# Kernel tuning notes

Measured on AMD Instinct MI355X. Metric: run time of the kernel, lower is better.

Reference implementation:

```python
import jax, jax.numpy as jnp
import numpy as np

HDIM = 1024
CDIM = 256
TEMPER = 10.0
IGNORE_OUT = 0.0
EPS = 1e-6


def setup_inputs() -> dict:
    key = jax.random.key(0)
    ks = jax.random.split(key, 6)
    B, T, D = 2, 128, 384
    x = jax.random.normal(ks[0], (B, T, D), jnp.float32)
    y = jax.random.normal(ks[1], (B, T, D), jnp.float32)
    # xavier-normal style init for the two linear layers
    W_enc = jax.random.normal(ks[2], (D, HDIM), jnp.float32) * np.sqrt(2.0 / (D + HDIM))
    b_enc = jnp.zeros((HDIM,), jnp.float32)
    W_dec = jax.random.normal(ks[3], (HDIM, D), jnp.float32) * np.sqrt(2.0 / (D + HDIM))
    b_dec = jnp.zeros((D,), jnp.float32)
    return {"x": x, "y": y, "W_enc": W_enc, "b_enc": b_enc, "W_dec": W_dec, "b_dec": b_dec}


def reference(x, y, W_enc, b_enc, W_dec, b_dec):
    B, T, D = x.shape
    n_iter = HDIM // CDIM
    pad = D - 1
    # shift_idx[s, j] = s + j : window of width D at offset s, s in [0, 2D-2]
    shift_idx = jnp.arange(2 * D - 1)[:, None] + jnp.arange(D)[None, :]

    seq_mask = (y == IGNORE_OUT)                       # (B,T,D) bool
    denom_seq = jnp.sum(~seq_mask).astype(x.dtype)
    qn = jnp.linalg.norm(y, axis=-1)                   # (B,T)

    mask_prev = None
    x_dis, losses = [], []
    for _ in range(n_iter):
        # --- _pad_for_shift: (B,T,2D-1,D) shifted windows of x ---
        kp = jnp.pad(x, ((0, 0), (0, 0), (pad, pad)))  # (B,T,3D-2)
        kpt = kp[..., shift_idx]                       # (B,T,2D-1,D)
        # --- _score (cos) + argmax over shifts ---
        kn = jnp.linalg.norm(kpt, axis=-1)             # (B,T,2D-1)
        sim = jnp.einsum('btsd,btd->bts', kpt, y) / (qn[..., None] * kn + EPS)
        sim = jnp.where(jnp.isnan(sim), 0.0, sim)
        theta = jnp.argmax(sim, axis=-1)               # (B,T) int
        x_opt = jnp.take_along_axis(kpt, theta[..., None, None], axis=-2)[..., 0, :]  # (B,T,D)
        # --- attention: elementwise cos-scaled score, temp softmax, detached ---
        dn = (jnp.linalg.norm(x_opt, axis=-1, keepdims=True)
              * jnp.linalg.norm(y, axis=-1, keepdims=True) + EPS)
        attn = jax.nn.softmax((x_opt * y / dn) / TEMPER, axis=-1)
        attn = jnp.where(jnp.isnan(attn), 0.0, attn)
        attn = jax.lax.stop_gradient(attn)
        x_attn = x_opt * attn
        # --- _reverse_pad_for_shift: window at offset 2D-2-theta ---
        kp2 = jnp.pad(x_attn, ((0, 0), (0, 0), (pad, pad)))
        rev_idx = (2 * D - 2 - theta)[..., None] + jnp.arange(D)  # (B,T,D)
        x_ele = jnp.take_along_axis(kp2, rev_idx, axis=-1)         # (B,T,D)
        # --- self_net: encoder -> top-k sparsify -> decoder_self ---
        h = x_ele @ W_enc + b_enc                      # (B,T,HDIM)
        if mask_prev is not None:
            h = jnp.where(mask_prev > 0, 1e-10, h)
        _, idx_top = jax.lax.top_k(h, CDIM)            # (B,T,CDIM)
        flat = idx_top.reshape(B * T, CDIM)
        mask_cur = jnp.zeros((B * T, HDIM), x.dtype).at[
            jnp.arange(B * T)[:, None], flat].set(1.0).reshape(B, T, HDIM)
        if mask_prev is None:
            mask_prev = mask_cur
        else:
            mask_prev = mask_prev + mask_cur - mask_prev * mask_cur
        h = h * mask_cur
        out = h @ W_dec + b_dec                        # (B,T,D)
        x_dis.append(out)
        # --- SeqLoss (masked MSE, mean-reduced by count of valid elems) ---
        err = jnp.where(seq_mask, 0.0, (out - x) ** 2) / denom_seq
        losses.append(jnp.sum(err))
    return jnp.stack(x_dis), jnp.stack(losses)
```

## Files before the change

### kernel.cpp

```cpp
#include <hip/hip_runtime.h>
#include <math.h>

#define DD 384
#define HD 1024
#define CD 256
#define NS 765
#define NITER 4
#define NROWS 256
#define TEMPER_F 10.0f
#define EPSF 1e-6f
#define CUTF 1e-10f

typedef unsigned long long u64;
typedef unsigned int u32;

__device__ __forceinline__ u32 flipf(float f) {
    u32 u = __float_as_uint(f);
    return u ^ ((u32)((int)u >> 31) | 0x80000000u);
}
__device__ __forceinline__ float unflipf(u32 s) {
    u32 fl = ~s;
    u32 u = (fl & 0x80000000u) ? (fl ^ 0x80000000u) : ~fl;
    return __uint_as_float(u);
}
__device__ __forceinline__ u64 shflx64(u64 v, int m) {
    int lo = __shfl_xor((int)(u32)v, m, 64);
    int hi = __shfl_xor((int)(u32)(v >> 32), m, 64);
    return ((u64)(u32)hi << 32) | (u32)lo;
}
__device__ __forceinline__ u32 bf16r(float f) {
    u32 u = __float_as_uint(f);
    return (u + 0x7FFFu + ((u >> 16) & 1u)) >> 16;
}
__device__ __forceinline__ u32 pack2(float a, float b) {
    return bf16r(a) | (bf16r(b) << 16);
}
__device__ __forceinline__ float blo(u32 p) { return __uint_as_float(p << 16); }
__device__ __forceinline__ float bhi(u32 p) { return __uint_as_float(p & 0xFFFF0000u); }

__global__ __launch_bounds__(256) void convert_kernel(
    const float* __restrict__ We, const float* __restrict__ Wd,
    uint2* __restrict__ we16, uint2* __restrict__ wd16)
{
    const int t = blockIdx.x * 256 + threadIdx.x;
    for (int i = t; i < (DD * HD) / 4; i += 65536) {
        float4 v = ((const float4*)We)[i];
        we16[i] = make_uint2(pack2(v.x, v.y), pack2(v.z, v.w));
    }
    for (int i = t; i < (HD * DD) / 4; i += 65536) {
        float4 v = ((const float4*)Wd)[i];
        wd16[i] = make_uint2(pack2(v.x, v.y), pack2(v.z, v.w));
    }
}

__global__ __launch_bounds__(512) void fused_kernel(
    const float* __restrict__ x, const float* __restrict__ y,
    const u32* __restrict__ wenc16, const float* __restrict__ benc,
    const u32* __restrict__ wdec16, const float* __restrict__ bdec,
    float* __restrict__ out_xdis, float* __restrict__ lossp,
    int* __restrict__ ycnt)
{
    const int row  = blockIdx.x;
    const int tid  = threadIdx.x;
    const int lane = tid & 63;
    const int wid  = tid >> 6;

    __shared__ __align__(16) float xpad[1152];
    __shared__ __align__(16) float yr[DD];
    __shared__ float xa[DD];
    __shared__ __align__(16) float xe_s[DD];
    __shared__ __align__(16) float hpart[HD];
    __shared__ __align__(16) u64   skey[HD];
    __shared__ __align__(16) uint2 dec2[HD];
    __shared__ float wred[8];
    __shared__ int   wredi[8];
    __shared__ float wredn[8];
    __shared__ float s_sc[4];
    __shared__ int   s_theta, s_fb;
    __shared__ float loss4[NITER];

    const float* xrow = x + row * DD;
    const float* yrow = y + row * DD;

    for (int i = tid; i < 1152; i += 512)
        xpad[i] = (i >= DD - 1 && i < 2 * DD - 1) ? xrow[i - (DD - 1)] : 0.f;
    if (tid < DD) yr[tid] = yrow[tid];
    __syncthreads();

    if (tid < DD) {
        float p = yr[tid] * yr[tid];
        int   c = (yr[tid] != 0.f) ? 1 : 0;
        for (int o = 32; o; o >>= 1) {
            p += __shfl_xor(p, o, 64);
            c += __shfl_xor(c, o, 64);
        }
        if (lane == 0) { wred[wid] = p; wredi[wid] = c; }
    }
    __syncthreads();
    if (tid == 0) {
        float s = 0.f; int c = 0;
        for (int w = 0; w < 6; ++w) { s += wred[w]; c += wredi[w]; }
        s_sc[0] = sqrtf(s);
        ycnt[row] = c;
    }
    __syncthreads();
    const float qn = s_sc[0];

    float bv = -INFINITY; int bs = 0x7fffffff; float bn = 0.f;
    if (tid < 192) {
        const float4* xp4 = (const float4*)xpad;
        const float4* yp4 = (const float4*)yr;
        float4 A = xp4[tid];
        const float f0 = A.x * A.x, f1 = A.y * A.y, f2 = A.z * A.z;
        float d0 = 0.f, d1 = 0.f, d2 = 0.f, d3 = 0.f, n0 = 0.f;
#pragma unroll 4
        for (int jc = 0; jc < 96; ++jc) {
            float4 B = xp4[tid + jc + 1];
            float4 Y = yp4[jc];
            d0 += A.x * Y.x; d0 += A.y * Y.y; d0 += A.z * Y.z; d0 += A.w * Y.w;
            d1 += A.y * Y.x; d1 += A.z * Y.y; d1 += A.w * Y.z; d1 += B.x * Y.w;
            d2 += A.z * Y.x; d2 += A.w * Y.y; d2 += B.x * Y.z; d2 += B.y * Y.w;
            d3 += A.w * Y.x; d3 += B.x * Y.y; d3 += B.y * Y.z; d3 += B.z * Y.w;
            n0 += A.x * A.x; n0 += A.y * A.y; n0 += A.z * A.z; n0 += A.w * A.w;
            A = B;
        }
        const float n1 = n0 - f0 + A.x * A.x;
        const float n2 = n1 - f1 + A.y * A.y;
        const float n3 = n2 - f2 + A.z * A.z;
        const int s0 = 4 * tid;
        float sim0 = d0 / (qn * sqrtf(n0) + EPSF);
        float sim1 = d1 / (qn * sqrtf(n1) + EPSF);
        float sim2 = d2 / (qn * sqrtf(n2) + EPSF);
        float sim3 = d3 / (qn * sqrtf(n3) + EPSF);
        bv = sim0; bs = s0; bn = n0;
        if (s0 + 1 < NS && sim1 > bv) { bv = sim1; bs = s0 + 1; bn = n1; }
        if (s0 + 2 < NS && sim2 > bv) { bv = sim2; bs = s0 + 2; bn = n2; }
        if (s0 + 3 < NS && sim3 > bv) { bv = sim3; bs = s0 + 3; bn = n3; }
    }
    for (int o = 32; o; o >>= 1) {
        float v2 = __shfl_xor(bv, o, 64);
        int   i2 = __shfl_xor(bs, o, 64);
        float n2 = __shfl_xor(bn, o, 64);
        if (v2 > bv || (v2 == bv && i2 < bs)) { bv = v2; bs = i2; bn = n2; }
    }
    if (lane == 0) { wred[wid] = bv; wredi[wid] = bs; wredn[wid] = bn; }
    __syncthreads();
    if (tid == 0) {
        float v = wred[0]; int b = wredi[0]; float nn = wredn[0];
        for (int w = 1; w < 8; ++w)
            if (wred[w] > v || (wred[w] == v && wredi[w] < b)) {
                v = wred[w]; b = wredi[w]; nn = wredn[w];
            }
        s_theta = b;
        s_sc[1] = sqrtf(nn) * qn + EPSF;
    }
    __syncthreads();
    const int theta = s_theta;
    const float dn = s_sc[1];

    float xo = 0.f, z = 0.f;
    if (tid < DD) {
        xo = xpad[theta + tid];
        z = (xo * yr[tid] / dn) / TEMPER_F;
        float m = z;
        for (int o = 32; o; o >>= 1) { float w2 = __shfl_xor(m, o, 64); if (w2 > m) m = w2; }
        if (lane == 0) wred[wid] = m;
    }
    __syncthreads();
    if (tid == 0) {
        float m = wred[0];
        for (int w = 1; w < 6; ++w) if (wred[w] > m) m = wred[w];
        s_sc[2] = m;
    }
    __syncthreads();
    float ez = 0.f;
    if (tid < DD) {
        ez = expf(z - s_sc[2]);
        float p = ez;
        for (int o = 32; o; o >>= 1) p += __shfl_xor(p, o, 64);
        if (lane == 0) wred[wid] = p;
    }
    __syncthreads();
    if (tid == 0) {
        float s = 0.f;
        for (int w = 0; w < 6; ++w) s += wred[w];
        s_sc[3] = s;
    }
    __syncthreads();
    if (tid < DD) xa[tid] = xo * (ez / s_sc[3]);
    __syncthreads();
    if (tid < DD) {
        int sj = tid - (theta - (DD - 1));
        xe_s[tid] = (sj >= 0 && sj < DD) ? xa[sj] : 0.f;
    }
    __syncthreads();

    const int c4 = tid & 255;
    const int jh = tid >> 8;
    float4 acc = make_float4(0.f, 0.f, 0.f, 0.f);
    {
        const u32* wbase = wenc16 + (size_t)(jh * 192) * 512 + 2 * c4;
        const float* xb = xe_s + jh * 192;
#pragma unroll 8
        for (int j = 0; j < 192; ++j) {
            float xv = xb[j];
            uint2 wv = *(const uint2*)(wbase + (size_t)j * 512);
            acc.x += xv * blo(wv.x); acc.y += xv * bhi(wv.x);
            acc.z += xv * blo(wv.y); acc.w += xv * bhi(wv.y);
        }
    }
    if (jh == 1) *(float4*)&hpart[4 * c4] = acc;
    if (tid == 0) s_fb = HD;
    if (tid < NITER) loss4[tid] = 0.f;
    __syncthreads();
    if (jh == 0) {
        float4 hp = *(const float4*)&hpart[4 * c4];
        float4 bb = *(const float4*)&benc[4 * c4];
        hp.x += acc.x + bb.x;
        hp.y += acc.y + bb.y;
        hp.z += acc.z + bb.z;
        hp.w += acc.w + bb.w;
        *(float4*)&hpart[4 * c4] = hp;
    }
    __syncthreads();

    float2 hh = *(const float2*)&hpart[2 * tid];
    u64 e0 = ((u64)(~flipf(hh.x)) << 32) | (u32)(2 * tid);
    u64 e1 = ((u64)(~flipf(hh.y)) << 32) | (u32)(2 * tid + 1);

    for (int k = 2; k <= HD; k <<= 1) {
        const bool up = ((2 * tid) & k) == 0;
        for (int j = k >> 1; j > 0; j >>= 1) {
            if (j == 1) {
                bool sw = up ? (e0 > e1) : (e0 < e1);
                if (sw) { u64 t2 = e0; e0 = e1; e1 = t2; }
            } else if (j <= 64) {
                const int m = j >> 1;
                u64 p0 = shflx64(e0, m);
                u64 p1 = shflx64(e1, m);
                const bool takeMin = (((tid & m) == 0) == up);
                e0 = takeMin ? (e0 < p0 ? e0 : p0) : (e0 > p0 ? e0 : p0);
                e1 = takeMin ? (e1 < p1 ? e1 : p1) : (e1 > p1 ? e1 : p1);
            } else {
                __syncthreads();
                skey[2 * tid]     = e0;
                skey[2 * tid + 1] = e1;
                __syncthreads();
                const int tp = tid ^ (j >> 1);
                u64 p0 = skey[2 * tp];
                u64 p1 = skey[2 * tp + 1];
                const bool takeMin = (((tid & (j >> 1)) == 0) == up);
                e0 = takeMin ? (e0 < p0 ? e0 : p0) : (e0 > p0 ? e0 : p0);
                e1 = takeMin ? (e1 < p1 ? e1 : p1) : (e1 > p1 ? e1 : p1);
            }
        }
    }

    {
        float v0 = unflipf((u32)(e0 >> 32));
        float v1 = unflipf((u32)(e1 >> 32));
        dec2[2 * tid]     = make_uint2(__float_as_uint(v0), ((u32)e0) * 192);
        dec2[2 * tid + 1] = make_uint2(__float_as_uint(v1), ((u32)e1) * 192);
        int fbloc = HD;
        if (!(v1 > CUTF)) fbloc = 2 * tid + 1;
        if (!(v0 > CUTF)) fbloc = 2 * tid;
        for (int o = 32; o; o >>= 1) { int t2 = __shfl_xor(fbloc, o, 64); if (t2 < fbloc) fbloc = t2; }
        if (lane == 0) atomicMin(&s_fb, fbloc);
    }
    __syncthreads();
    const int fb = s_fb;

    {
        const int k = tid >> 7;
        const int g = tid & 127;
        const bool active = (g < 96);
        int n = 0;
        if (active) {
            n = (k == 0) ? CD : fb - k * CD;
            if (n < 0) n = 0; if (n > CD) n = CD;
        }
        float4 oacc = make_float4(0.f, 0.f, 0.f, 0.f);
        if (active) oacc = *(const float4*)&bdec[4 * g];
        const u32* wd = wdec16 + 2 * g;
        const int base = k * CD;
        int r = 0;
        for (; r + 8 <= n; r += 8) {
#pragma unroll
            for (int q = 0; q < 8; q += 2) {
                uint4 dv = *(const uint4*)&dec2[base + r + q];
                float v0 = __uint_as_float(dv.x);
                uint2 w0 = *(const uint2*)(wd + dv.y);
                float v1 = __uint_as_float(dv.z);
                uint2 w1 = *(const uint2*)(wd + dv.w);
                oacc.x += v0 * blo(w0.x); oacc.y += v0 * bhi(w0.x);
                oacc.z += v0 * blo(w0.y); oacc.w += v0 * bhi(w0.y);
                oacc.x += v1 * blo(w1.x); oacc.y += v1 * bhi(w1.x);
                oacc.z += v1 * blo(w1.y); oacc.w += v1 * bhi(w1.y);
            }
        }
        for (; r < n; ++r) {
            uint2 dv = dec2[base + r];
            float v0 = __uint_as_float(dv.x);
            uint2 w0 = *(const uint2*)(wd + dv.y);
            oacc.x += v0 * blo(w0.x); oacc.y += v0 * bhi(w0.x);
            oacc.z += v0 * blo(w0.y); oacc.w += v0 * bhi(w0.y);
        }
        float l = 0.f;
        if (active) {
            *(float4*)&out_xdis[((size_t)k * NROWS + row) * DD + 4 * g] = oacc;
            float4 xv = *(const float4*)&xrow[4 * g];
            float4 yv = *(const float4*)&yr[4 * g];
            float e;
            e = oacc.x - xv.x; if (yv.x != 0.f) l += e * e;
            e = oacc.y - xv.y; if (yv.y != 0.f) l += e * e;
            e = oacc.z - xv.z; if (yv.z != 0.f) l += e * e;
            e = oacc.w - xv.w; if (yv.w != 0.f) l += e * e;
        }
        for (int o = 32; o; o >>= 1) l += __shfl_xor(l, o, 64);
        if (lane == 0) atomicAdd(&loss4[k], l);
    }
    __syncthreads();
    if (tid < NITER) lossp[row * NITER + tid] = loss4[tid];
}

__global__ __launch_bounds__(256) void finalize2(
    const float* __restrict__ lossp, const int* __restrict__ ycnt,
    float* __restrict__ losses)
{
    const int tid = threadIdx.x, lane = tid & 63, w = tid >> 6;
    __shared__ int ctot[4];
    int c = ycnt[tid];
    for (int o = 32; o; o >>= 1) c += __shfl_xor(c, o, 64);
    if (lane == 0) ctot[w] = c;
    __syncthreads();
    const int total = ctot[0] + ctot[1] + ctot[2] + ctot[3];
    float s = lossp[lane * NITER + w] + lossp[(lane + 64) * NITER + w]
            + lossp[(lane + 128) * NITER + w] + lossp[(lane + 192) * NITER + w];
    for (int o = 32; o; o >>= 1) s += __shfl_xor(s, o, 64);
    if (lane == 0) losses[w] = s / (float)total;
}

extern "C" void kernel_launch(void* const* d_in, const int* in_sizes, int n_in,
                              void* d_out, int out_size, void* d_ws, size_t ws_size,
                              hipStream_t stream) {
    const float* x    = (const float*)d_in[0];
    const float* y    = (const float*)d_in[1];
    const float* Wenc = (const float*)d_in[2];
    const float* benc = (const float*)d_in[3];
    const float* Wdec = (const float*)d_in[4];
    const float* bdec = (const float*)d_in[5];

    float* out  = (float*)d_out;
    float* loss = out + (out_size - NITER);

    float* lossp  = (float*)d_ws;
    int*   ycnt   = (int*)(lossp + NROWS * NITER);
    u32*   wenc16 = (u32*)(ycnt + NROWS);
    u32*   wdec16 = wenc16 + (DD * HD) / 2;

    convert_kernel<<<256, 256, 0, stream>>>(Wenc, Wdec, (uint2*)wenc16, (uint2*)wdec16);
    fused_kernel<<<NROWS, 512, 0, stream>>>(x, y, wenc16, benc, wdec16, bdec,
                                            out, lossp, ycnt);
    finalize2<<<1, 256, 0, stream>>>(lossp, ycnt, loss);
}
```

Before: 111.3 us.

## Double block size to 1024 threads, splitting encoder K and sort per element

Launches the fused per-row kernel with 1024 threads instead of 512. The encoder matvec splits K into four 96-long slices reduced through shared memory, the bitonic top-k sort holds one key per thread instead of two, and the decoder gives each thread two output columns instead of four. The aim is more parallelism per row, since only 256 blocks run on a large GPU and per-thread serial work dominates. In exchange there are more barriers, more shared-memory reduction traffic and higher register pressure under the 1024-thread launch bound. Parts of the sort-stage code and the argmax reduction setup are not visible, so whether every phase was adjusted for 16 wavefronts cannot be confirmed.

```diff
diff --git a/kernel.cpp b/kernel.cpp
--- a/kernel.cpp
+++ b/kernel.cpp
@@ -53,7 +53,7 @@
     }
 }
 
-__global__ __launch_bounds__(512) void fused_kernel(
+__global__ __launch_bounds__(1024) void fused_kernel(
     const float* __restrict__ x, const float* __restrict__ y,
     const u32* __restrict__ wenc16, const float* __restrict__ benc,
     const u32* __restrict__ wdec16, const float* __restrict__ bdec,
@@ -69,12 +69,12 @@
     __shared__ __align__(16) float yr[DD];
     __shared__ float xa[DD];
     __shared__ __align__(16) float xe_s[DD];
-    __shared__ __align__(16) float hpart[HD];
+    __shared__ __align__(16) float part[4][HD];
     __shared__ __align__(16) u64   skey[HD];
     __shared__ __align__(16) uint2 dec2[HD];
-    __shared__ float wred[8];
-    __shared__ int   wredi[8];
-    __shared__ float wredn[8];
+    __shared__ float wred[16];
+    __shared__ int   wredi[16];
+    __shared__ float wredn[16];
     __shared__ float s_sc[4];
     __shared__ int   s_theta, s_fb;
     __shared__ float loss4[NITER];
@@ -82,7 +82,7 @@
     const float* xrow = x + row * DD;
     const float* yrow = y + row * DD;
 
-    for (int i = tid; i < 1152; i += 512)
+    for (int i = tid; i < 1152; i += 1024)
         xpad[i] = (i >= DD - 1 && i < 2 * DD - 1) ? xrow[i - (DD - 1)] : 0.f;
     if (tid < DD) yr[tid] = yrow[tid];
     __syncthreads();
@@ -147,7 +147,7 @@
     __syncthreads();
     if (tid == 0) {
         float v = wred[0]; int b = wredi[0]; float nn = wredn[0];
-        for (int w = 1; w < 8; ++w)
+        for (int w = 1; w < 16; ++w)
             if (wred[w] > v || (wred[w] == v && wredi[w] < b)) {
                 v = wred[w]; b = wredi[w]; nn = wredn[w];
             }
@@ -195,75 +195,54 @@
     }
     __syncthreads();
 
-    const int c4 = tid & 255;
-    const int jh = tid >> 8;
-    float4 acc = make_float4(0.f, 0.f, 0.f, 0.f);
     {
-        const u32* wbase = wenc16 + (size_t)(jh * 192) * 512 + 2 * c4;
-        const float* xb = xe_s + jh * 192;
+        const int ks = tid >> 8;
+        const int c4 = tid & 255;
+        const u32* wbase = wenc16 + (size_t)(ks * 96) * 512 + 2 * c4;
+        const float* xb = xe_s + ks * 96;
+        float4 acc = make_float4(0.f, 0.f, 0.f, 0.f);
 #pragma unroll 8
-        for (int j = 0; j < 192; ++j) {
+        for (int j = 0; j < 96; ++j) {
             float xv = xb[j];
             uint2 wv = *(const uint2*)(wbase + (size_t)j * 512);
             acc.x += xv * blo(wv.x); acc.y += xv * bhi(wv.x);
             acc.z += xv * blo(wv.y); acc.w += xv * bhi(wv.y);
         }
-    }
-    if (jh == 1) *(float4*)&hpart[4 * c4] = acc;
+        *(float4*)&part[ks][4 * c4] = acc;
+    }
     if (tid == 0) s_fb = HD;
     if (tid < NITER) loss4[tid] = 0.f;
     __syncthreads();
-    if (jh == 0) {
-        float4 hp = *(const float4*)&hpart[4 * c4];
-        float4 bb = *(const float4*)&benc[4 * c4];
-        hp.x += acc.x + bb.x;
-        hp.y += acc.y + bb.y;
-        hp.z += acc.z + bb.z;
-        hp.w += acc.w + bb.w;
-        *(float4*)&hpart[4 * c4] = hp;
-    }
-    __syncthreads();
-
-    float2 hh = *(const float2*)&hpart[2 * tid];
-    u64 e0 = ((u64)(~flipf(hh.x)) << 32) | (u32)(2 * tid);
-    u64 e1 = ((u64)(~flipf(hh.y)) << 32) | (u32)(2 * tid + 1);
+
+    u64 e;
+    {
+        float hv = part[0][tid] + part[1][tid] + part[2][tid] + part[3][tid]
+                 + benc[tid];
+        e = ((u64)(~flipf(hv)) << 32) | (u32)tid;
+    }
 
     for (int k = 2; k <= HD; k <<= 1) {
-        const bool up = ((2 * tid) & k) == 0;
+        const bool up = (tid & k) == 0;
         for (int j = k >> 1; j > 0; j >>= 1) {
-            if (j == 1) {
-                bool sw = up ? (e0 > e1) : (e0 < e1);
-                if (sw) { u64 t2 = e0; e0 = e1; e1 = t2; }
-            } else if (j <= 64) {
-                const int m = j >> 1;
-                u64 p0 = shflx64(e0, m);
-                u64 p1 = shflx64(e1, m);
-                const bool takeMin = (((tid & m) == 0) == up);
-                e0 = takeMin ? (e0 < p0 ? e0 : p0) : (e0 > p0 ? e0 : p0);
-                e1 = takeMin ? (e1 < p1 ? e1 : p1) : (e1 > p1 ? e1 : p1);
+            if (j <= 32) {
+                u64 p = shflx64(e, j);
+                const bool takeMin = ((tid & j) == 0) == up;
+                e = takeMin ? (e < p ? e : p) : (e > p ? e : p);
             } else {
                 __syncthreads();
-                skey[2 * tid]     = e0;
-                skey[2 * tid + 1] = e1;
+                skey[tid] = e;
                 __syncthreads();
-                const int tp = tid ^ (j >> 1);
-                u64 p0 = skey[2 * tp];
-                u64 p1 = skey[2 * tp + 1];
-                const bool takeMin = (((tid & (j >> 1)) == 0) == up);
-                e0 = takeMin ? (e0 < p0 ? e0 : p0) : (e0 > p0 ? e0 : p0);
-                e1 = takeMin ? (e1 < p1 ? e1 : p1) : (e1 > p1 ? e1 : p1);
+                u64 p = skey[tid ^ j];
+                const bool takeMin = ((tid & j) == 0) == up;
+                e = takeMin ? (e < p ? e : p) : (e > p ? e : p);
             }
         }
     }
 
     {
-        float v0 = unflipf((u32)(e0 >> 32));
-        float v1 = unflipf((u32)(e1 >> 32));
-        dec2[2 * tid]     = make_uint2(__float_as_uint(v0), ((u32)e0) * 192);
-        dec2[2 * tid + 1] = make_uint2(__float_as_uint(v1), ((u32)e1) * 192);
-        int fbloc = HD;
-        if (!(v1 > CUTF)) fbloc = 2 * tid + 1;
-        if (!(v0 > CUTF)) fbloc = 2 * tid;
+        float v = unflipf((u32)(e >> 32));
+        dec2[tid] = make_uint2(__float_as_uint(v), ((u32)e) * 192);
+        int fbloc = (v > CUTF) ? HD : tid;
         for (int o = 32; o; o >>= 1) { int t2 = __shfl_xor(fbloc, o, 64); if (t2 < fbloc) fbloc = t2; }
         if (lane == 0) atomicMin(&s_fb, fbloc);
     }
@@ -271,17 +250,17 @@
     const int fb = s_fb;
 
     {
-        const int k = tid >> 7;
-        const int g = tid & 127;
-        const bool active = (g < 96);
+        const int k = tid >> 8;
+        const int g = tid & 255;
+        const bool active = (g < 192);
         int n = 0;
         if (active) {
             n = (k == 0) ? CD : fb - k * CD;
             if (n < 0) n = 0; if (n > CD) n = CD;
         }
-        float4 oacc = make_float4(0.f, 0.f, 0.f, 0.f);
-        if (active) oacc = *(const float4*)&bdec[4 * g];
-        const u32* wd = wdec16 + 2 * g;
+        float2 oacc = make_float2(0.f, 0.f);
+        if (active) oacc = *(const float2*)&bdec[2 * g];
+        const u32* wd = wdec16 + g;
         const int base = k * CD;
         int r = 0;
         for (; r + 8 <= n; r += 8) {
@@ -289,32 +268,27 @@
             for (int q = 0; q < 8; q += 2) {
                 uint4 dv = *(const uint4*)&dec2[base + r + q];
                 float v0 = __uint_as_float(dv.x);
-                uint2 w0 = *(const uint2*)(wd + dv.y);
+                u32 w0 = wd[dv.y];
                 float v1 = __uint_as_float(dv.z);
-                uint2 w1 = *(const uint2*)(wd + dv.w);
-                oacc.x += v0 * blo(w0.x); oacc.y += v0 * bhi(w0.x);
-                oacc.z += v0 * blo(w0.y); oacc.w += v0 * bhi(w0.y);
-                oacc.x += v1 * blo(w1.x); oacc.y += v1 * bhi(w1.x);
-                oacc.z += v1 * blo(w1.y); oacc.w += v1 * bhi(w1.y);
+                u32 w1 = wd[dv.w];
+                oacc.x += v0 * blo(w0); oacc.y += v0 * bhi(w0);
+                oacc.x += v1 * blo(w1); oacc.y += v1 * bhi(w1);
             }
         }
         for (; r < n; ++r) {
             uint2 dv = dec2[base + r];
             float v0 = __uint_as_float(dv.x);
-            uint2 w0 = *(const uint2*)(wd + dv.y);
-            oacc.x += v0 * blo(w0.x); oacc.y += v0 * bhi(w0.x);
-            oacc.z += v0 * blo(w0.y); oacc.w += v0 * bhi(w0.y);
+            u32 w0 = wd[dv.y];
+            oacc.x += v0 * blo(w0); oacc.y += v0 * bhi(w0);
         }
         float l = 0.f;
         if (active) {
-            *(float4*)&out_xdis[((size_t)k * NROWS + row) * DD + 4 * g] = oacc;
-            float4 xv = *(const float4*)&xrow[4 * g];
-            float4 yv = *(const float4*)&yr[4 * g];
-            float e;
-            e = oacc.x - xv.x; if (yv.x != 0.f) l += e * e;
-            e = oacc.y - xv.y; if (yv.y != 0.f) l += e * e;
-            e = oacc.z - xv.z; if (yv.z != 0.f) l += e * e;
-            e = oacc.w - xv.w; if (yv.w != 0.f) l += e * e;
+            *(float2*)&out_xdis[((size_t)k * NROWS + row) * DD + 2 * g] = oacc;
+            float2 xv = *(const float2*)&xrow[2 * g];
+            float2 yv = *(const float2*)&yr[2 * g];
+            float ee;
+            ee = oacc.x - xv.x; if (yv.x != 0.f) l += ee * ee;
+            ee = oacc.y - xv.y; if (yv.y != 0.f) l += ee * ee;
         }
         for (int o = 32; o; o >>= 1) l += __shfl_xor(l, o, 64);
         if (lane == 0) atomicAdd(&loss4[k], l);
@@ -359,7 +333,7 @@
     u32*   wdec16 = wenc16 + (DD * HD) / 2;
 
     convert_kernel<<<256, 256, 0, stream>>>(Wenc, Wdec, (uint2*)wenc16, (uint2*)wdec16);
-    fused_kernel<<<NROWS, 512, 0, stream>>>(x, y, wenc16, benc, wdec16, bdec,
-                                            out, lossp, ycnt);
+    fused_kernel<<<NROWS, 1024, 0, stream>>>(x, y, wenc16, benc, wdec16, bdec,
+                                             out, lossp, ycnt);
     finalize2<<<1, 256, 0, stream>>>(lossp, ycnt, loss);
 }
```

Result: no change. 109.8 us (-1.4%).
